# Performance work log

Hardware: AMD Instinct MI355X
Metric: run time of the kernel (lower is better)

## Reference

```python
import jax, jax.numpy as jnp
import numpy as np

B, DIN, DH, DOUT = 4096, 512, 1024, 256
DFF = 4 * DH
STEPS = 30
REF_DIM = 64
GAMMA = 0.5 * min(1.0, float(np.sqrt(REF_DIM / DIN)))  # dimension-scaled gamma
LN_EPS = 1e-5


def setup_inputs() -> dict:
    key = jax.random.key(0)
    ks = jax.random.split(key, 6)
    rn = lambda k, shp, s: (jax.random.normal(k, shp, jnp.float32) * s)
    return {
        "x": rn(ks[0], (B, DIN), 1.0),
        "embed_w": rn(ks[1], (DH, DIN), 0.02),
        "embed_b": jnp.zeros((DH,), jnp.float32),
        "W1": rn(ks[2], (DFF, DH), 0.02),
        "b1": jnp.zeros((DFF,), jnp.float32),
        "W2": rn(ks[3], (DH, DFF), 0.02),
        "b2": jnp.zeros((DH,), jnp.float32),
        "ln_g": jnp.ones((DH,), jnp.float32),
        "ln_b": jnp.zeros((DH,), jnp.float32),
        "head_w": rn(ks[4], (DOUT, DH), 0.02),
        "head_b": jnp.zeros((DOUT,), jnp.float32),
    }


def _spectral_normalize(W, n_iter=15):
    # power iteration (u, v treated as constants, like torch spectral_norm buffers)
    v0 = jnp.full((W.shape[1],), 1.0 / np.sqrt(W.shape[1]), W.dtype)
    def body(i, uv):
        _, v = uv
        u = W @ v
        u = u / (jnp.linalg.norm(u) + 1e-12)
        v = W.T @ u
        v = v / (jnp.linalg.norm(v) + 1e-12)
        return (u, v)
    u0 = W @ v0
    u0 = u0 / (jnp.linalg.norm(u0) + 1e-12)
    u, v = jax.lax.fori_loop(0, n_iter, body, (u0, v0))
    u = jax.lax.stop_gradient(u)
    v = jax.lax.stop_gradient(v)
    sigma = u @ (W @ v)  # grad flows through W here, as in torch
    return W / sigma


def _layernorm(h, g, b):
    mu = jnp.mean(h, axis=-1, keepdims=True)
    var = jnp.var(h, axis=-1, keepdims=True)
    return (h - mu) * jax.lax.rsqrt(var + LN_EPS) * g + b


def reference(x, embed_w, embed_b, W1, b1, W2, b2, ln_g, ln_b, head_w, head_b):
    W1n = _spectral_normalize(W1)
    W2n = _spectral_normalize(W2)
    x_emb = x @ embed_w.T + embed_b  # [B, DH]; constant across steps

    def ffn(h):
        hn = _layernorm(h, ln_g, ln_b)
        hid = jnp.tanh(hn @ W1n.T + b1)  # dropout p=0 -> identity
        return hid @ W2n.T + b2

    def step(h, _):
        h_target = ffn(h) + x_emb
        h_next = (1.0 - GAMMA) * h + GAMMA * h_target
        return h_next, None

    h, _ = jax.lax.scan(step, x_emb, None, length=STEPS)
    return h @ head_w.T + head_b
```

## Files before the change

### kernel.cpp

```cpp
#include <hip/hip_runtime.h>
#include <hip/hip_bf16.h>
#include <math.h>

#define B_    4096
#define DIN_  512
#define DH_   1024
#define DOUT_ 256
#define DFF_  4096
#define STEPS_ 30
#define GAMMA_ 0.17677669529663687f
#define LN_EPS_ 1e-5f

typedef __attribute__((ext_vector_type(8))) short short8;
typedef __attribute__((ext_vector_type(4))) float f32x4;

__device__ inline void gload_lds16(const void* g, void* l) {
  __builtin_amdgcn_global_load_lds(
      (const __attribute__((address_space(1))) unsigned int*)g,
      (__attribute__((address_space(3))) unsigned int*)l, 16, 0, 0);
}

__device__ inline float fast_tanh(float v) {
  const float e = __expf(2.f * v);
  return 1.f - 2.f * __builtin_amdgcn_rcpf(e + 1.f);
}

__device__ inline float bf2f(unsigned short u) {
  return __uint_as_float((unsigned)u << 16);
}

__global__ __launch_bounds__(512, 2) void gemm256(
    const __hip_bfloat16* __restrict__ A, const __hip_bfloat16* __restrict__ Bm,
    int M, int N, int K, int kc, int nt, const float* __restrict__ bias,
    int epi, __hip_bfloat16* __restrict__ bf16out) {
  __shared__ __align__(16) char lds[2][65536];
  const int tid = threadIdx.x;
  const int lane = tid & 63;
  const int wid = tid >> 6;
  const int wr = wid >> 2;
  const int wc = wid & 3;

  const int gx = gridDim.x;
  const int nwg = gx * gridDim.y;
  const int wg = blockIdx.y * gx + blockIdx.x;
  const int cpx = nwg >> 3;
  const int swz = (wg & 7) * cpx + (wg >> 3);
  const int bx = swz % gx, by = swz / gx;
  const int m0 = by * 256, n0 = bx * 256;
  const int zk = blockIdx.z * kc;

  const int u = (lane < 32) ? lane : (lane ^ 2);
  const int rr = u >> 3;
  const int ccb = (u & 7) * 8;

  f32x4 acc[8][4];
  const f32x4 zero = {0.f, 0.f, 0.f, 0.f};
#pragma unroll
  for (int i = 0; i < 8; ++i)
#pragma unroll
    for (int j = 0; j < 4; ++j) acc[i][j] = zero;

  auto STAGE = [&](int t, int buf) {
    const int kt = zk + t * 64;
#pragma unroll
    for (int j = 0; j < 8; ++j) {
      const int c = wid * 8 + j;
      const int cm = c & 31;
      const int row = cm * 8 + rr;
      const __hip_bfloat16* src =
          (c < 32) ? A + (size_t)(m0 + row) * K + kt + ccb
                   : Bm + (size_t)(n0 + row) * K + kt + ccb;
      gload_lds16((const void*)src, (void*)(&lds[buf][c * 1024]));
    }
  };

  STAGE(0, 0);
  STAGE(1, 1);

  const int ar = lane & 15;
  const int kq = (lane >> 4) * 16;
  const int brow0 = (wc & 1) * 64;

  for (int t = 0; t < nt; ++t) {
    const int buf = t & 1;
    if (t == nt - 1) {
      asm volatile("s_waitcnt vmcnt(0)" ::: "memory");
    } else {
      asm volatile("s_waitcnt vmcnt(8)" ::: "memory");
    }
    __builtin_amdgcn_s_barrier();
    __builtin_amdgcn_sched_barrier(0);

    const char* Ah = &lds[buf][wr * 16384];
    const char* Bh = &lds[buf][32768 + (wc >> 1) * 16384];
#pragma unroll
    for (int ks = 0; ks < 2; ++ks) {
      short8 av[8], bv[4];
#pragma unroll
      for (int mf = 0; mf < 8; ++mf) {
        int off = (mf * 16 + ar) * 128 + ks * 64 + kq;
        off ^= ((off >> 9) & 1) << 5;
        av[mf] = *(const short8*)(Ah + off);
      }
#pragma unroll
      for (int nf = 0; nf < 4; ++nf) {
        int off = (brow0 + nf * 16 + ar) * 128 + ks * 64 + kq;
        off ^= ((off >> 9) & 1) << 5;
        bv[nf] = *(const short8*)(Bh + off);
      }
      __builtin_amdgcn_s_setprio(1);
#pragma unroll
      for (int mf = 0; mf < 8; ++mf)
#pragma unroll
        for (int nf = 0; nf < 4; ++nf)
          acc[mf][nf] = __builtin_amdgcn_mfma_f32_16x16x32_bf16(av[mf], bv[nf], acc[mf][nf], 0, 0, 0);
      __builtin_amdgcn_s_setprio(0);
    }

    __builtin_amdgcn_sched_barrier(0);
    __builtin_amdgcn_s_barrier();
    __builtin_amdgcn_sched_barrier(0);
    if (t + 2 < nt) STAGE(t + 2, buf);
  }

  if (epi == 4) bf16out += (size_t)blockIdx.z * ((size_t)M * N);
  const int rb = (lane >> 4) * 4;
#pragma unroll
  for (int mf = 0; mf < 8; ++mf) {
#pragma unroll
    for (int nf = 0; nf < 4; ++nf) {
      const int col = n0 + wc * 64 + nf * 16 + ar;
      const float bvs = bias ? bias[col] : 0.f;
#pragma unroll
      for (int j = 0; j < 4; ++j) {
        const int row = m0 + wr * 128 + mf * 16 + rb + j;
        float v = acc[mf][nf][j] + bvs;
        if (epi == 1) v = fast_tanh(v);
        bf16out[(size_t)row * N + col] = __float2bfloat16(v);
      }
    }
  }
}

__global__ __launch_bounds__(256) void gemm_bt(
    const __hip_bfloat16* __restrict__ A, const __hip_bfloat16* __restrict__ Bm,
    int M, int N, int K, const float* __restrict__ bias, int epi,
    float* __restrict__ f32out, float* __restrict__ f32out2) {
  __shared__ __align__(16) short As[128 * 32];
  __shared__ __align__(16) short Bs[128 * 32];
  const int tid = threadIdx.x;
  const int lane = tid & 63;
  const int wid = tid >> 6;
  const int wr = wid >> 1, wc = wid & 1;

  const int gx = gridDim.x;
  const int nwg = gx * gridDim.y;
  const int wg = blockIdx.y * gx + blockIdx.x;
  const int cpx = nwg >> 3;
  const int swz = (wg & 7) * cpx + (wg >> 3);
  const int bx = swz % gx, by = swz / gx;

  const int m0 = by * 128, n0 = bx * 128;
  const int ldsrow = lane >> 2;
  const int col8 = (lane & 3) * 8;

  f32x4 acc[4][4];
  const f32x4 zero = {0.f, 0.f, 0.f, 0.f};
#pragma unroll
  for (int i = 0; i < 4; ++i)
#pragma unroll
    for (int j = 0; j < 4; ++j) acc[i][j] = zero;

  for (int kt = 0; kt < K; kt += 32) {
#pragma unroll
    for (int i = 0; i < 2; ++i) {
      const int seg = wid * 2 + i;
      gload_lds16(A + (size_t)(m0 + seg * 16 + ldsrow) * K + kt + col8,
                  (void*)(As + seg * 512));
      gload_lds16(Bm + (size_t)(n0 + seg * 16 + ldsrow) * K + kt + col8,
                  (void*)(Bs + seg * 512));
    }
    __syncthreads();
    short8 a[4], b[4];
#pragma unroll
    for (int mf = 0; mf < 4; ++mf)
      a[mf] = *(const short8*)&As[(wr * 64 + mf * 16 + (lane & 15)) * 32 + (lane >> 4) * 8];
#pragma unroll
    for (int nf = 0; nf < 4; ++nf)
      b[nf] = *(const short8*)&Bs[(wc * 64 + nf * 16 + (lane & 15)) * 32 + (lane >> 4) * 8];
#pragma unroll
    for (int mf = 0; mf < 4; ++mf)
#pragma unroll
      for (int nf = 0; nf < 4; ++nf)
        acc[mf][nf] = __builtin_amdgcn_mfma_f32_16x16x32_bf16(a[mf], b[nf], acc[mf][nf], 0, 0, 0);
    __syncthreads();
  }

  const int rbase = (lane >> 4) * 4;
  const int cin = lane & 15;
#pragma unroll
  for (int mf = 0; mf < 4; ++mf) {
#pragma unroll
    for (int nf = 0; nf < 4; ++nf) {
      const int col = n0 + wc * 64 + nf * 16 + cin;
      const float bv = bias[col];
#pragma unroll
      for (int j = 0; j < 4; ++j) {
        const int row = m0 + wr * 64 + mf * 16 + rbase + j;
        const float v = acc[mf][nf][j] + bv;
        const size_t idx = (size_t)row * N + col;
        if (epi == 0) {
          f32out[idx] = v;
          f32out2[idx] = v;
        } else {
          f32out[idx] = v;
        }
      }
    }
  }
}

__global__ __launch_bounds__(256) void reduce_ln_kernel(
    const __hip_bfloat16* __restrict__ ps, const float* __restrict__ b2,
    const float* __restrict__ xe, float* __restrict__ h,
    const float* __restrict__ g, const float* __restrict__ be,
    __hip_bfloat16* __restrict__ outbf, int do_ln) {
  const int row = blockIdx.x, tid = threadIdx.x;
  const size_t base = (size_t)row * DH_;
  const size_t slab = (size_t)B_ * DH_;
  float pv0 = 0.f, pv1 = 0.f, pv2 = 0.f, pv3 = 0.f;
#pragma unroll
  for (int z = 0; z < 4; ++z) {
    const ushort4 q = ((const ushort4*)(ps + z * slab + base))[tid];
    pv0 += bf2f(q.x); pv1 += bf2f(q.y); pv2 += bf2f(q.z); pv3 += bf2f(q.w);
  }
  const float4 xv = ((const float4*)(xe + base))[tid];
  const float4 hv = ((const float4*)(h + base))[tid];
  const float4 bv = ((const float4*)b2)[tid];
  float4 nv;
  nv.x = (1.f - GAMMA_) * hv.x + GAMMA_ * (pv0 + bv.x + xv.x);
  nv.y = (1.f - GAMMA_) * hv.y + GAMMA_ * (pv1 + bv.y + xv.y);
  nv.z = (1.f - GAMMA_) * hv.z + GAMMA_ * (pv2 + bv.z + xv.z);
  nv.w = (1.f - GAMMA_) * hv.w + GAMMA_ * (pv3 + bv.w + xv.w);
  ((float4*)(h + base))[tid] = nv;

  __hip_bfloat16* out = outbf + base + tid * 4;
  if (!do_ln) {
    out[0] = __float2bfloat16(nv.x);
    out[1] = __float2bfloat16(nv.y);
    out[2] = __float2bfloat16(nv.z);
    out[3] = __float2bfloat16(nv.w);
    return;
  }
  float s = nv.x + nv.y + nv.z + nv.w;
  float ss = nv.x * nv.x + nv.y * nv.y + nv.z * nv.z + nv.w * nv.w;
#pragma unroll
  for (int o = 32; o > 0; o >>= 1) {
    s += __shfl_down(s, o, 64);
    ss += __shfl_down(ss, o, 64);
  }
  __shared__ float rs_[4], rss_[4];
  const int lane = tid & 63, wid = tid >> 6;
  if (lane == 0) { rs_[wid] = s; rss_[wid] = ss; }
  __syncthreads();
  const float tot = rs_[0] + rs_[1] + rs_[2] + rs_[3];
  const float tots = rss_[0] + rss_[1] + rss_[2] + rss_[3];
  const float mu = tot * (1.f / DH_);
  const float var = tots * (1.f / DH_) - mu * mu;
  const float rstd = rsqrtf(var + LN_EPS_);
  const float4 gv = ((const float4*)g)[tid];
  const float4 bev = ((const float4*)be)[tid];
  out[0] = __float2bfloat16((nv.x - mu) * rstd * gv.x + bev.x);
  out[1] = __float2bfloat16((nv.y - mu) * rstd * gv.y + bev.y);
  out[2] = __float2bfloat16((nv.z - mu) * rstd * gv.z + bev.z);
  out[3] = __float2bfloat16((nv.w - mu) * rstd * gv.w + bev.w);
}

__global__ __launch_bounds__(256) void ln_cast_kernel(
    const float* __restrict__ h, const float* __restrict__ g,
    const float* __restrict__ be, __hip_bfloat16* __restrict__ hn) {
  const int row = blockIdx.x;
  const int tid = threadIdx.x;
  const float4 v = ((const float4*)(h + (size_t)row * DH_))[tid];
  float s = v.x + v.y + v.z + v.w;
  float ss = v.x * v.x + v.y * v.y + v.z * v.z + v.w * v.w;
#pragma unroll
  for (int o = 32; o > 0; o >>= 1) {
    s += __shfl_down(s, o, 64);
    ss += __shfl_down(ss, o, 64);
  }
  __shared__ float rs_[4], rss_[4];
  const int lane = tid & 63, wid = tid >> 6;
  if (lane == 0) { rs_[wid] = s; rss_[wid] = ss; }
  __syncthreads();
  const float tot = rs_[0] + rs_[1] + rs_[2] + rs_[3];
  const float tots = rss_[0] + rss_[1] + rss_[2] + rss_[3];
  const float mu = tot * (1.f / DH_);
  const float var = tots * (1.f / DH_) - mu * mu;
  const float rstd = rsqrtf(var + LN_EPS_);
  const float4 gv = ((const float4*)g)[tid];
  const float4 bv = ((const float4*)be)[tid];
  __hip_bfloat16* out = hn + (size_t)row * DH_ + tid * 4;
  out[0] = __float2bfloat16((v.x - mu) * rstd * gv.x + bv.x);
  out[1] = __float2bfloat16((v.y - mu) * rstd * gv.y + bv.y);
  out[2] = __float2bfloat16((v.z - mu) * rstd * gv.z + bv.z);
  out[3] = __float2bfloat16((v.w - mu) * rstd * gv.w + bv.w);
}

__global__ __launch_bounds__(256) void matvec2_kernel(
    const float* __restrict__ Wa, const float* __restrict__ xa,
    float* __restrict__ ya, int rowsA, int colsA,
    const float* __restrict__ Wb, const float* __restrict__ xb,
    float* __restrict__ yb, int rowsB, int colsB) {
  const int gw = (int)(blockIdx.x * 256 + threadIdx.x) >> 6;
  const int lane = threadIdx.x & 63;
  const float* W;
  const float* x;
  float* y;
  int row, cols;
  if (gw < rowsA) {
    W = Wa; x = xa; y = ya; row = gw; cols = colsA;
  } else {
    row = gw - rowsA;
    if (row >= rowsB) return;
    W = Wb; x = xb; y = yb; cols = colsB;
  }
  const float4* wr = (const float4*)(W + (size_t)row * cols);
  const float4* xv = (const float4*)x;
  const int n4 = cols >> 2;
  float s = 0.f;
  for (int c = lane; c < n4; c += 64) {
    const float4 wv = wr[c];
    const float4 vv = xv[c];
    s += wv.x * vv.x + wv.y * vv.y + wv.z * vv.z + wv.w * vv.w;
  }
#pragma unroll
  for (int o = 32; o > 0; o >>= 1) s += __shfl_down(s, o, 64);
  if (lane == 0) y[row] = s;
}

__global__ __launch_bounds__(256) void transpose_kernel(
    const float* __restrict__ in, float* __restrict__ out, int R, int C) {
  __shared__ float t[32][33];
  const int lx = threadIdx.x & 31, ly = threadIdx.x >> 5;
  const int r0 = blockIdx.y * 32, c0 = blockIdx.x * 32;
#pragma unroll
  for (int j = 0; j < 32; j += 8) t[ly + j][lx] = in[(size_t)(r0 + ly + j) * C + c0 + lx];
  __syncthreads();
#pragma unroll
  for (int j = 0; j < 32; j += 8) out[(size_t)(c0 + ly + j) * R + r0 + lx] = t[lx][ly + j];
}

__global__ void init_v_kernel(float* v1, float* v2) {
  const int i = blockIdx.x * 256 + threadIdx.x;
  if (i < 1024) v1[i] = 0.03125f;
  if (i < 4096) v2[i] = 0.015625f;
}

__global__ __launch_bounds__(256) void cast_kernel(
    const float* __restrict__ s, __hip_bfloat16* __restrict__ d, int n) {
  const int b = (blockIdx.x * 256 + threadIdx.x) * 4;
  if (b < n) {
    const float4 v = *(const float4*)(s + b);
    d[b] = __float2bfloat16(v.x);
    d[b + 1] = __float2bfloat16(v.y);
    d[b + 2] = __float2bfloat16(v.z);
    d[b + 3] = __float2bfloat16(v.w);
  }
}

__global__ __launch_bounds__(256) void cast_scaled_kernel(
    const float* __restrict__ s, __hip_bfloat16* __restrict__ d, int n,
    const float* __restrict__ rs) {
  const float r = rs[0];
  const int b = (blockIdx.x * 256 + threadIdx.x) * 4;
  if (b < n) {
    const float4 v = *(const float4*)(s + b);
    d[b] = __float2bfloat16(v.x * r);
    d[b + 1] = __float2bfloat16(v.y * r);
    d[b + 2] = __float2bfloat16(v.z * r);
    d[b + 3] = __float2bfloat16(v.w * r);
  }
}

__global__ __launch_bounds__(256) void sigma_rs_kernel(
    const float* __restrict__ c, int m, const float* __restrict__ dv, int n,
    float* __restrict__ rs) {
  const int tid = threadIdx.x;
  float sc = 0.f, sd = 0.f;
  for (int i = tid; i < m; i += 256) { const float v = c[i]; sc += v * v; }
  for (int i = tid; i < n; i += 256) { const float v = dv[i]; sd += v * v; }
#pragma unroll
  for (int o = 32; o > 0; o >>= 1) {
    sc += __shfl_down(sc, o, 64);
    sd += __shfl_down(sd, o, 64);
  }
  __shared__ float a[4], b[4];
  const int lane = tid & 63, wid = tid >> 6;
  if (lane == 0) { a[wid] = sc; b[wid] = sd; }
  __syncthreads();
  if (tid == 0) {
    const float tc = a[0] + a[1] + a[2] + a[3];
    const float td = b[0] + b[1] + b[2] + b[3];
    rs[0] = sqrtf(tc / td);
  }
}

extern "C" void kernel_launch(void* const* d_in, const int* in_sizes, int n_in,
                              void* d_out, int out_size, void* d_ws, size_t ws_size,
                              hipStream_t stream) {
  const float* x       = (const float*)d_in[0];
  const float* embed_w = (const float*)d_in[1];
  const float* embed_b = (const float*)d_in[2];
  const float* W1      = (const float*)d_in[3];
  const float* b1      = (const float*)d_in[4];
  const float* W2      = (const float*)d_in[5];
  const float* b2      = (const float*)d_in[6];
  const float* ln_g    = (const float*)d_in[7];
  const float* ln_b    = (const float*)d_in[8];
  const float* head_w  = (const float*)d_in[9];
  const float* head_b  = (const float*)d_in[10];
  float* out = (float*)d_out;

  char* p = (char*)d_ws;
  auto carve = [&](size_t bytes) {
    char* r = p;
    p += (bytes + 255) & ~(size_t)255;
    return (void*)r;
  };
  float* h     = (float*)carve((size_t)B_ * DH_ * 4);
  float* x_emb = (float*)carve((size_t)B_ * DH_ * 4);
  float* W1T   = (float*)carve((size_t)DFF_ * DH_ * 4);
  float* W2T   = (float*)carve((size_t)DH_ * DFF_ * 4);
  __hip_bfloat16* ps = (__hip_bfloat16*)W1T;
  __hip_bfloat16* hn   = (__hip_bfloat16*)carve((size_t)B_ * DH_ * 2);
  __hip_bfloat16* hid  = (__hip_bfloat16*)carve((size_t)B_ * DFF_ * 2);
  __hip_bfloat16* W1n  = (__hip_bfloat16*)carve((size_t)DFF_ * DH_ * 2);
  __hip_bfloat16* W2n  = (__hip_bfloat16*)carve((size_t)DH_ * DFF_ * 2);
  __hip_bfloat16* xbf  = (__hip_bfloat16*)carve((size_t)B_ * DIN_ * 2);
  __hip_bfloat16* ewbf = (__hip_bfloat16*)carve((size_t)DH_ * DIN_ * 2);
  __hip_bfloat16* hwbf = (__hip_bfloat16*)carve((size_t)DOUT_ * DH_ * 2);
  __hip_bfloat16* hbf  = (__hip_bfloat16*)carve((size_t)B_ * DH_ * 2);
  float* v1a = (float*)carve(4096 * 4);
  float* v1b = (float*)carve(4096 * 4);
  float* c1  = (float*)carve(4096 * 4);
  float* v2a = (float*)carve(4096 * 4);
  float* v2b = (float*)carve(4096 * 4);
  float* c2  = (float*)carve(4096 * 4);
  float* rs1 = (float*)carve(256);
  float* rs2 = (float*)carve(256);

  transpose_kernel<<<dim3(DH_ / 32, DFF_ / 32), 256, 0, stream>>>(W1, W1T, DFF_, DH_);
  transpose_kernel<<<dim3(DFF_ / 32, DH_ / 32), 256, 0, stream>>>(W2, W2T, DH_, DFF_);
  init_v_kernel<<<16, 256, 0, stream>>>(v1a, v2a);
  cast_kernel<<<(B_ * DIN_ / 4) / 256, 256, 0, stream>>>(x, xbf, B_ * DIN_);
  cast_kernel<<<(DH_ * DIN_ / 4) / 256, 256, 0, stream>>>(embed_w, ewbf, DH_ * DIN_);
  cast_kernel<<<(DOUT_ * DH_ / 4) / 256, 256, 0, stream>>>(head_w, hwbf, DOUT_ * DH_);

  gemm_bt<<<dim3(DH_ / 128, B_ / 128), 256, 0, stream>>>(
      xbf, ewbf, B_, DH_, DIN_, embed_b, 0, x_emb, h);

  for (int it = 0; it < 15; ++it) {
    const float* vin1 = (it & 1) ? v1b : v1a;
    float* vout1 = (it & 1) ? v1a : v1b;
    const float* vin2 = (it & 1) ? v2b : v2a;
    float* vout2 = (it & 1) ? v2a : v2b;
    matvec2_kernel<<<((DFF_ + DH_) * 64) / 256, 256, 0, stream>>>(
        W1, vin1, c1, DFF_, DH_, W2, vin2, c2, DH_, DFF_);
    matvec2_kernel<<<((DH_ + DFF_) * 64) / 256, 256, 0, stream>>>(
        W1T, c1, vout1, DH_, DFF_, W2T, c2, vout2, DFF_, DH_);
  }
  sigma_rs_kernel<<<1, 256, 0, stream>>>(c1, DFF_, v1b, DH_, rs1);
  sigma_rs_kernel<<<1, 256, 0, stream>>>(c2, DH_, v2b, DFF_, rs2);
  cast_scaled_kernel<<<(DFF_ * DH_ / 4) / 256, 256, 0, stream>>>(W1, W1n, DFF_ * DH_, rs1);
  cast_scaled_kernel<<<(DH_ * DFF_ / 4) / 256, 256, 0, stream>>>(W2, W2n, DH_ * DFF_, rs2);

  ln_cast_kernel<<<B_, 256, 0, stream>>>(h, ln_g, ln_b, hn);

  for (int s = 0; s < STEPS_; ++s) {
    gemm256<<<dim3(DFF_ / 256, B_ / 256, 1), 512, 0, stream>>>(
        hn, W1n, B_, DFF_, DH_, DH_, DH_ / 64, b1, 1, hid);
    gemm256<<<dim3(DH_ / 256, B_ / 256, 4), 512, 0, stream>>>(
        hid, W2n, B_, DH_, DFF_, DFF_ / 4, DFF_ / 4 / 64, nullptr, 4, ps);
    const int last = (s == STEPS_ - 1);
    reduce_ln_kernel<<<B_, 256, 0, stream>>>(
        ps, b2, x_emb, h, ln_g, ln_b, last ? hbf : hn, last ? 0 : 1);
  }

  gemm_bt<<<dim3(DOUT_ / 128, B_ / 128), 256, 0, stream>>>(
      hbf, hwbf, B_, DOUT_, DH_, head_b, 3, out, nullptr);
}
```

Baseline: 3.527 ms.

## Switch gemm256 to 4-stage K=32 LDS pipeline with single barrier per step

Replaces the double-buffered 64-wide K tile with four 32-wide K stages kept in flight, issuing the next global-to-LDS load right after fragments are read into registers. This removes the second per-iteration barrier and the XOR-swizzled LDS addressing, and is meant to hide more memory latency behind the MFMAs. The unswizzled 64-byte row stride may cause LDS bank conflicts, and half-size K steps double the barrier count per tile.

```diff
diff --git a/kernel.cpp b/kernel.cpp
--- a/kernel.cpp
+++ b/kernel.cpp
@@ -33,7 +33,7 @@
     const __hip_bfloat16* __restrict__ A, const __hip_bfloat16* __restrict__ Bm,
     int M, int N, int K, int kc, int nt, const float* __restrict__ bias,
     int epi, __hip_bfloat16* __restrict__ bf16out) {
-  __shared__ __align__(16) char lds[2][65536];
+  __shared__ __align__(16) char lds[4][32768];
   const int tid = threadIdx.x;
   const int lane = tid & 63;
   const int wid = tid >> 6;
@@ -49,9 +49,8 @@
   const int m0 = by * 256, n0 = bx * 256;
   const int zk = blockIdx.z * kc;
 
-  const int u = (lane < 32) ? lane : (lane ^ 2);
-  const int rr = u >> 3;
-  const int ccb = (u & 7) * 8;
+  const int srow = wid * 16 + (lane >> 2);
+  const int scol = (lane & 3) * 8;
 
   f32x4 acc[8][4];
   const f32x4 zero = {0.f, 0.f, 0.f, 0.f};
@@ -60,67 +59,57 @@
 #pragma unroll
     for (int j = 0; j < 4; ++j) acc[i][j] = zero;
 
-  auto STAGE = [&](int t, int buf) {
-    const int kt = zk + t * 64;
-#pragma unroll
-    for (int j = 0; j < 8; ++j) {
-      const int c = wid * 8 + j;
-      const int cm = c & 31;
-      const int row = cm * 8 + rr;
+  auto STAGE = [&](int t) {
+    const int kt = zk + t * 32;
+    char* base = &lds[t & 3][0];
+#pragma unroll
+    for (int q = 0; q < 4; ++q) {
       const __hip_bfloat16* src =
-          (c < 32) ? A + (size_t)(m0 + row) * K + kt + ccb
-                   : Bm + (size_t)(n0 + row) * K + kt + ccb;
-      gload_lds16((const void*)src, (void*)(&lds[buf][c * 1024]));
+          (q < 2) ? A + (size_t)(m0 + q * 128 + srow) * K + kt + scol
+                  : Bm + (size_t)(n0 + (q - 2) * 128 + srow) * K + kt + scol;
+      gload_lds16((const void*)src, (void*)(base + q * 8192 + wid * 1024));
     }
   };
 
-  STAGE(0, 0);
-  STAGE(1, 1);
+  STAGE(0);
+  STAGE(1);
+  STAGE(2);
 
   const int ar = lane & 15;
-  const int kq = (lane >> 4) * 16;
-  const int brow0 = (wc & 1) * 64;
+  const int hb = (lane >> 4) * 16;
 
   for (int t = 0; t < nt; ++t) {
-    const int buf = t & 1;
-    if (t == nt - 1) {
+    const char* base = &lds[t & 3][0];
+    if (t + 3 <= nt) {
+      asm volatile("s_waitcnt vmcnt(8)" ::: "memory");
+    } else if (t + 2 == nt) {
+      asm volatile("s_waitcnt vmcnt(4)" ::: "memory");
+    } else {
       asm volatile("s_waitcnt vmcnt(0)" ::: "memory");
-    } else {
-      asm volatile("s_waitcnt vmcnt(8)" ::: "memory");
     }
     __builtin_amdgcn_s_barrier();
     __builtin_amdgcn_sched_barrier(0);
 
-    const char* Ah = &lds[buf][wr * 16384];
-    const char* Bh = &lds[buf][32768 + (wc >> 1) * 16384];
-#pragma unroll
-    for (int ks = 0; ks < 2; ++ks) {
-      short8 av[8], bv[4];
-#pragma unroll
-      for (int mf = 0; mf < 8; ++mf) {
-        int off = (mf * 16 + ar) * 128 + ks * 64 + kq;
-        off ^= ((off >> 9) & 1) << 5;
-        av[mf] = *(const short8*)(Ah + off);
-      }
-#pragma unroll
-      for (int nf = 0; nf < 4; ++nf) {
-        int off = (brow0 + nf * 16 + ar) * 128 + ks * 64 + kq;
-        off ^= ((off >> 9) & 1) << 5;
-        bv[nf] = *(const short8*)(Bh + off);
-      }
-      __builtin_amdgcn_s_setprio(1);
-#pragma unroll
-      for (int mf = 0; mf < 8; ++mf)
-#pragma unroll
-        for (int nf = 0; nf < 4; ++nf)
-          acc[mf][nf] = __builtin_amdgcn_mfma_f32_16x16x32_bf16(av[mf], bv[nf], acc[mf][nf], 0, 0, 0);
-      __builtin_amdgcn_s_setprio(0);
-    }
-
+    short8 av[8], bv[4];
+#pragma unroll
+    for (int mf = 0; mf < 8; ++mf)
+      av[mf] = *(const short8*)(base + (wr * 128 + mf * 16 + ar) * 64 + hb);
+#pragma unroll
+    for (int nf = 0; nf < 4; ++nf)
+      bv[nf] = *(const short8*)(base + 16384 + (wc * 64 + nf * 16 + ar) * 64 + hb);
+
+    if (t + 3 < nt) STAGE(t + 3);
+
+    asm volatile("s_waitcnt lgkmcnt(0)" ::: "memory");
     __builtin_amdgcn_sched_barrier(0);
-    __builtin_amdgcn_s_barrier();
+    __builtin_amdgcn_s_setprio(1);
+#pragma unroll
+    for (int mf = 0; mf < 8; ++mf)
+#pragma unroll
+      for (int nf = 0; nf < 4; ++nf)
+        acc[mf][nf] = __builtin_amdgcn_mfma_f32_16x16x32_bf16(av[mf], bv[nf], acc[mf][nf], 0, 0, 0);
+    __builtin_amdgcn_s_setprio(0);
     __builtin_amdgcn_sched_barrier(0);
-    if (t + 2 < nt) STAGE(t + 2, buf);
   }
 
   if (epi == 4) bf16out += (size_t)blockIdx.z * ((size_t)M * N);
@@ -479,9 +468,9 @@
 
   for (int s = 0; s < STEPS_; ++s) {
     gemm256<<<dim3(DFF_ / 256, B_ / 256, 1), 512, 0, stream>>>(
-        hn, W1n, B_, DFF_, DH_, DH_, DH_ / 64, b1, 1, hid);
+        hn, W1n, B_, DFF_, DH_, DH_, DH_ / 32, b1, 1, hid);
     gemm256<<<dim3(DH_ / 256, B_ / 256, 4), 512, 0, stream>>>(
-        hid, W2n, B_, DH_, DFF_, DFF_ / 4, DFF_ / 4 / 64, nullptr, 4, ps);
+        hid, W2n, B_, DH_, DFF_, DFF_ / 4, DFF_ / 4 / 32, nullptr, 4, ps);
     const int last = (s == STEPS_ - 1);
     reduce_ln_kernel<<<B_, 256, 0, stream>>>(
         ps, b2, x_emb, h, ln_g, ln_b, last ? hbf : hn, last ? 0 : 1);
```

New measurement: 3.340 ms. 5.3% less time.
